# Optimization experiments

Hardware: AMD Instinct MI355X
Metric: run time of the kernel (lower is better)

Reference implementation:

```python
import jax, jax.numpy as jnp
import numpy as np

C = 1024        # number of classes
N = 8           # proxies per class
ALLNUM = C * N  # 8192 total proxies
DIM = 512
R = 0.05
TOPK = int(np.ceil(R * ALLNUM))  # 410
LAM = 0.3
B = 2048


def setup_inputs() -> dict:
    key = jax.random.key(0)
    k1, k2, k3 = jax.random.split(key, 3)
    inp = jax.random.normal(k1, (B, DIM), dtype=jnp.float32)
    target = jax.random.randint(k2, (B,), 0, C, dtype=jnp.int64)
    # kaiming-uniform-initialized proxies approximated by scaled normal init
    proxies = jax.random.normal(k3, (DIM, ALLNUM), dtype=jnp.float32)
    instance_label = jnp.repeat(jnp.arange(C, dtype=jnp.int64), N)  # [ALLNUM]
    return {"input": inp, "target": target, "Proxies": proxies,
            "instance_label": instance_label}


def reference(input, target, Proxies, instance_label):
    # L2-normalize each proxy column (F.normalize along dim=0, eps=1e-12)
    norm = jnp.maximum(jnp.linalg.norm(Proxies, axis=0, keepdims=True), 1e-12)
    centers = Proxies / norm                             # [DIM, ALLNUM]
    similarity = input @ centers                          # [B, ALLNUM]

    positive_mask = (target[:, None] == instance_label[None, :]).astype(similarity.dtype)
    _, indices = jax.lax.top_k(similarity + 1000.0 * positive_mask, TOPK)  # [B, TOPK]

    rows = jnp.arange(similarity.shape[0])[:, None]
    mask = jnp.zeros_like(similarity).at[rows, indices].set(1.0)
    prob_a = mask * similarity                            # sparse-masked similarities

    y_instance_onehot = jax.nn.one_hot(instance_label, C, dtype=similarity.dtype)  # [ALLNUM, C]
    logits = prob_a @ y_instance_onehot                   # [B, C]

    y_target_onehot = jax.nn.one_hot(target, C, dtype=similarity.dtype)  # [B, C]
    logits_mask = 1.0 - (logits == 0.0).astype(similarity.dtype)

    # scale_mask_softmax with scale=1 along dim=1
    e = jnp.exp(logits) * logits_mask
    predict = e / (1e-8 + jnp.sum(e, axis=1, keepdims=True))
    lossClassify = jnp.mean(jnp.sum(-y_target_onehot * jnp.log(predict + 1e-20), axis=1))

    # proxy regularizer: cross-entropy of proxy-vs-class logits
    simCenter = centers.T @ centers                       # [ALLNUM, ALLNUM]
    centers_logits = simCenter @ y_instance_onehot        # [ALLNUM, C]
    logp = jax.nn.log_softmax(centers_logits, axis=1)
    reg = -jnp.mean(jnp.take_along_axis(logp, instance_label[:, None], axis=1))

    return (lossClassify + LAM * reg, lossClassify)
```

## Files before the change

kernel.cpp:

```cpp
#include <hip/hip_runtime.h>
#include <hip/hip_bf16.h>
#include <math.h>

#define C_CLS   1024
#define NPROXY  8
#define ALLNUM  8192
#define DIM     512
#define TOPK    410
#define LAM     0.3f
#define BATCH   2048

#define BAND_CAP_BLK 40
#define ROW_CAP      512
#define GCAP         64

typedef __bf16 bf16x8 __attribute__((ext_vector_type(8)));
typedef float floatx4 __attribute__((ext_vector_type(4)));
typedef unsigned short ushort_t;

#define WS_RNORM 0
#define WS_SIG   8192
#define WS_LP    10240
#define WS_RP    12288
#define WS_CNT   14336
#define WS_NDEF  16384
#define WS_FLAG  18432
#define WS_CLS   20480
#define WS_BVAL  (WS_CLS + 2048*1024)
#define WS_BCOL  (WS_BVAL + 2048*512)
#define WS_ABF   (WS_BCOL + 2048*256)
#define WS_PBF   (WS_ABF + 524288)
#define WS_STBF  (WS_PBF + 2097152)
#define WS_LOG   (WS_STBF + 262144)

__device__ inline float block_reduce(float v, int is_max, float* red, int t) {
    #pragma unroll
    for (int o = 32; o > 0; o >>= 1) {
        float w = __shfl_down(v, o);
        v = is_max ? fmaxf(v, w) : (v + w);
    }
    __syncthreads();
    if ((t & 63) == 0) red[t >> 6] = v;
    __syncthreads();
    return is_max ? fmaxf(fmaxf(red[0], red[1]), fmaxf(red[2], red[3]))
                  : (red[0] + red[1] + red[2] + red[3]);
}

__device__ inline ushort_t f2bf(float f) {
    unsigned u = __float_as_uint(f);
    return (ushort_t)((u + 0x7FFFu + ((u >> 16) & 1u)) >> 16);
}

__device__ inline float bf2f(ushort_t u) {
    return __uint_as_float(((unsigned)u) << 16);
}

__device__ inline void ld_g2l_16(const void* g, void* l) {
    __builtin_amdgcn_global_load_lds(
        (const __attribute__((address_space(1))) unsigned int*)g,
        (__attribute__((address_space(3))) unsigned int*)l,
        16, 0, 0);
}

__device__ inline unsigned f2ord(float f) {
    unsigned u = __float_as_uint(f);
    return (u & 0x80000000u) ? ~u : (u | 0x80000000u);
}

__global__ __launch_bounds__(256) void k_prep1(const float* __restrict__ P,
                                               const float* __restrict__ input,
                                               float* __restrict__ rnorm,
                                               float* __restrict__ rowsig,
                                               ushort_t* __restrict__ Abf,
                                               ushort_t* __restrict__ Pbf,
                                               ushort_t* __restrict__ Stbf,
                                               unsigned* __restrict__ zaux) {
    __shared__ float tile[32][33];
    __shared__ float s_rn[32];
    float* cred = &tile[0][0];
    int bx = blockIdx.x, t = threadIdx.x;
    if (bx < 256) {
        int tc = t & 31, g = t >> 5;
        int c = bx * 32 + tc;
        const float* pc = P + (size_t)(g * 64) * ALLNUM + c;
        float s = 0.f;
        #pragma unroll 8
        for (int d = 0; d < 64; ++d) {
            float v = pc[(size_t)d * ALLNUM];
            s += v * v;
        }
        cred[g * 32 + tc] = s;
        __syncthreads();
        if (g == 0) {
            float tot = 0.f;
            #pragma unroll
            for (int k = 0; k < 8; ++k) tot += cred[k * 32 + tc];
            float r = 1.0f / fmaxf(sqrtf(tot), 1e-12f);
            rnorm[c] = r;
            s_rn[tc] = r;
        }
        __syncthreads();
        #pragma unroll
        for (int p = 0; p < 8; ++p) {
            int idx = t + 256 * p;
            int d = idx >> 2, cc = idx & 3;
            const float* pp = P + (size_t)d * ALLNUM + bx * 32 + cc * 8;
            const float* rr = &s_rn[cc * 8];
            float4 a = *(const float4*)pp;
            float4 b = *(const float4*)(pp + 4);
            float v = a.x * rr[0] + a.y * rr[1] + a.z * rr[2] + a.w * rr[3] +
                      b.x * rr[4] + b.y * rr[5] + b.z * rr[6] + b.w * rr[7];
            Stbf[(size_t)(bx * 4 + cc) * DIM + d] = f2bf(v);
        }
    } else if (bx < 256 + 1024) {
        int a = bx - 256;
        int idx = a * 256 + t;
        float4 v = ((const float4*)input)[idx];
        ushort4 o;
        o.x = f2bf(v.x); o.y = f2bf(v.y); o.z = f2bf(v.z); o.w = f2bf(v.w);
        ((ushort4*)Abf)[idx] = o;
        float sq = v.x * v.x + v.y * v.y + v.z * v.z + v.w * v.w;
        #pragma unroll
        for (int off = 32; off > 0; off >>= 1) sq += __shfl_down(sq, off);
        int lane = t & 63, w = t >> 6;
        if (lane == 0) cred[w] = sq;
        __syncthreads();
        if (t == 0) {
            rowsig[2 * a]     = sqrtf(cred[0] + cred[1]);
            rowsig[2 * a + 1] = sqrtf(cred[2] + cred[3]);
        }
    } else if (bx < 256 + 1024 + 4096) {
        int id = bx - 1280;
        int c0 = (id & 255) * 32, r0 = (id >> 8) * 32;
        int tc = t & 31, tr = t >> 5;
        #pragma unroll
        for (int p = 0; p < 4; ++p)
            tile[tr + p * 8][tc] = P[(size_t)(r0 + tr + p * 8) * ALLNUM + c0 + tc];
        __syncthreads();
        #pragma unroll
        for (int p = 0; p < 4; ++p) {
            int oc = tr + p * 8;
            Pbf[(size_t)(c0 + oc) * DIM + r0 + tc] = f2bf(tile[tc][oc]);
        }
    } else {
        for (int i = t; i < 3 * 2048; i += 256) zaux[i] = 0u;
    }
}

__global__ __launch_bounds__(512, 2) void k_gemms(const ushort_t* __restrict__ Abf,
                                                  const ushort_t* __restrict__ Pbf,
                                                  const ushort_t* __restrict__ Stbf,
                                                  const float* __restrict__ rnorm,
                                                  const float* __restrict__ rowsig,
                                                  const int* __restrict__ target,
                                                  float* __restrict__ g_cls,
                                                  float* __restrict__ g_bval,
                                                  ushort_t* __restrict__ g_bcol,
                                                  unsigned* __restrict__ g_cnt,
                                                  unsigned* __restrict__ g_ndef,
                                                  unsigned* __restrict__ g_flag,
                                                  ushort_t* __restrict__ logits) {
    __shared__ __align__(16) ushort_t smem[65536];
    int bx = blockIdx.x, t = threadIdx.x;
    int w = t >> 6, lane = t & 63;
    int ml = lane & 15, q4 = lane >> 4;

    if (bx < 256) {
        int bi = (bx >> 5) * 256, bj = (bx & 31) * 256;
        int wm = w >> 2, wn = w & 3;
        ushort_t* sA0 = smem;
        ushort_t* sB0 = smem + 16384;
        ushort_t* sA1 = smem + 32768;
        ushort_t* sB1 = smem + 49152;

        floatx4 acc[8][4];
        #pragma unroll
        for (int mf = 0; mf < 8; ++mf)
            #pragma unroll
            for (int nf = 0; nf < 4; ++nf)
                acc[mf][nf] = (floatx4){0.f, 0.f, 0.f, 0.f};

        #define STAGE0(sa, sb, k0) do {                                        \
            _Pragma("unroll")                                                  \
            for (int it = 0; it < 4; ++it) {                                   \
                int c = w * 256 + it * 64 + lane;                              \
                int m = c >> 3, s = c & 7, qq = s ^ (m & 7);                   \
                ld_g2l_16(Abf + ((size_t)(bi + m) << 9) + (k0) + qq * 8,       \
                          &(sa)[c * 8]);                                       \
            }                                                                  \
            _Pragma("unroll")                                                  \
            for (int it = 0; it < 4; ++it) {                                   \
                int c = w * 256 + it * 64 + lane;                              \
                int m = c >> 3, s = c & 7, qq = s ^ (m & 7);                   \
                ld_g2l_16(Pbf + ((size_t)(bj + m) << 9) + (k0) + qq * 8,       \
                          &(sb)[c * 8]);                                       \
            }                                                                  \
        } while (0)

        STAGE0(sA0, sB0, 0);
        __syncthreads();
        #pragma unroll
        for (int tt = 0; tt < 8; ++tt) {
            ushort_t* cA = (tt & 1) ? sA1 : sA0;
            ushort_t* cB = (tt & 1) ? sB1 : sB0;
            if (tt < 7) {
                if (tt & 1) STAGE0(sA0, sB0, (tt + 1) * 64);
                else        STAGE0(sA1, sB1, (tt + 1) * 64);
            }
            #pragma unroll
            for (int kk = 0; kk < 2; ++kk) {
                bf16x8 bfr[4];
                #pragma unroll
                for (int nf = 0; nf < 4; ++nf) {
                    int n = wn * 64 + nf * 16 + ml;
                    int s = (kk * 4 + q4) ^ (n & 7);
                    bfr[nf] = *(const bf16x8*)&cB[n * 64 + s * 8];
                }
                #pragma unroll
                for (int mf = 0; mf < 8; ++mf) {
                    int m = wm * 128 + mf * 16 + ml;
                    int s = (kk * 4 + q4) ^ (m & 7);
                    bf16x8 af = *(const bf16x8*)&cA[m * 64 + s * 8];
                    #pragma unroll
                    for (int nf = 0; nf < 4; ++nf)
                        acc[mf][nf] = __builtin_amdgcn_mfma_f32_16x16x32_bf16(
                            af, bfr[nf], acc[mf][nf], 0, 0, 0);
                }
            }
            __syncthreads();
        }

        unsigned char* sb8 = (unsigned char*)smem;
        float*    e_cls = (float*)sb8;
        float*    e_bv  = (float*)(sb8 + 32768);
        ushort_t* e_bc  = (ushort_t*)(sb8 + 73728);
        unsigned* e_cnt = (unsigned*)(sb8 + 94208);
        unsigned* e_nd  = (unsigned*)(sb8 + 95232);

        #pragma unroll
        for (int i = t; i < 8192; i += 512) e_cls[i] = 0.f;
        if (t < 256) { e_cnt[t] = 0u; e_nd[t] = 0u; }
        __syncthreads();

        #pragma unroll
        for (int mf = 0; mf < 8; ++mf) {
            int rl0 = wm * 128 + mf * 16 + q4 * 4;
            int rowb = bi + rl0;
            float4 rs4 = *(const float4*)&rowsig[rowb];
            int4   tg4 = *(const int4*)&target[rowb];
            #pragma unroll
            for (int nf = 0; nf < 4; ++nf) {
                int cl = wn * 64 + nf * 16 + ml;
                int col = bj + cl;
                float sc = rnorm[col];
                int cls = col >> 3;
                int clsl = cl >> 3;
                #pragma unroll
                for (int i = 0; i < 4; ++i) {
                    int rl = rl0 + i;
                    float v = acc[mf][nf][i] * sc;
                    float sg = ((const float*)&rs4)[i] * (1.0f / 22.616f);
                    float hiT = 1.80f * sg, loT = 1.47f * sg;
                    int tg = ((const int*)&tg4)[i];
                    if (cls == tg) {
                        atomicAdd(&e_cls[rl * 32 + clsl], v);
                    } else if (v >= hiT) {
                        atomicAdd(&e_cls[rl * 32 + clsl], v);
                        atomicAdd(&e_nd[rl], 1u);
                    } else if (v >= loT) {
                        unsigned u = atomicAdd(&e_cnt[rl], 1u);
                        if (u < BAND_CAP_BLK) {
                            e_bv[rl * BAND_CAP_BLK + u] = v;
                            e_bc[rl * BAND_CAP_BLK + u] = (ushort_t)col;
                        }
                    }
                }
            }
        }
        __syncthreads();

        int bjc = bj >> 3;
        #pragma unroll
        for (int i = t; i < 8192; i += 512) {
            int rl = i >> 5, c = i & 31;
            g_cls[(size_t)(bi + rl) * C_CLS + bjc + c] = e_cls[i];
        }
        if (t < 256) {
            int row = bi + t;
            unsigned cbb = e_cnt[t];
            unsigned nd = e_nd[t];
            if (nd) atomicAdd(&g_ndef[row], nd);
            if (cbb) {
                unsigned cc = (cbb > BAND_CAP_BLK) ? BAND_CAP_BLK : cbb;
                unsigned base = atomicAdd(&g_cnt[row], cc);
                if (cbb > BAND_CAP_BLK || base + cc > ROW_CAP) g_flag[row] = 1u;
                for (unsigned j = 0; j < cc; ++j) {
                    if (base + j >= ROW_CAP) break;
                    g_bval[(size_t)row * ROW_CAP + base + j] = e_bv[t * BAND_CAP_BLK + j];
                    g_bcol[(size_t)row * ROW_CAP + base + j] = e_bc[t * BAND_CAP_BLK + j];
                }
            }
        }
        #undef STAGE0
    } else {
        int id = bx - 256;
        int bi = (id >> 3) * 256, bj = (id & 7) * 128;
        int wm = w >> 1, wn = w & 1;
        ushort_t* sA0 = smem;
        ushort_t* sB0 = smem + 16384;
        ushort_t* sA1 = smem + 32768;
        ushort_t* sB1 = smem + 49152;

        floatx4 acc[4][4];
        #pragma unroll
        for (int mf = 0; mf < 4; ++mf)
            #pragma unroll
            for (int nf = 0; nf < 4; ++nf)
                acc[mf][nf] = (floatx4){0.f, 0.f, 0.f, 0.f};

        #define STAGE1(sa, sb, k0) do {                                        \
            _Pragma("unroll")                                                  \
            for (int it = 0; it < 4; ++it) {                                   \
                int c = w * 256 + it * 64 + lane;                              \
                int m = c >> 3, s = c & 7, qq = s ^ (m & 7);                   \
                ld_g2l_16(Pbf + ((size_t)(bi + m) << 9) + (k0) + qq * 8,       \
                          &(sa)[c * 8]);                                       \
            }                                                                  \
            _Pragma("unroll")                                                  \
            for (int it = 0; it < 2; ++it) {                                   \
                int c = w * 128 + it * 64 + lane;                              \
                int m = c >> 3, s = c & 7, qq = s ^ (m & 7);                   \
                ld_g2l_16(Stbf + ((size_t)(bj + m) << 9) + (k0) + qq * 8,      \
                          &(sb)[c * 8]);                                       \
            }                                                                  \
        } while (0)

        STAGE1(sA0, sB0, 0);
        __syncthreads();
        #pragma unroll
        for (int tt = 0; tt < 8; ++tt) {
            ushort_t* cA = (tt & 1) ? sA1 : sA0;
            ushort_t* cB = (tt & 1) ? sB1 : sB0;
            if (tt < 7) {
                if (tt & 1) STAGE1(sA0, sB0, (tt + 1) * 64);
                else        STAGE1(sA1, sB1, (tt + 1) * 64);
            }
            #pragma unroll
            for (int kk = 0; kk < 2; ++kk) {
                bf16x8 bfr[4];
                #pragma unroll
                for (int nf = 0; nf < 4; ++nf) {
                    int n = wn * 64 + nf * 16 + ml;
                    int s = (kk * 4 + q4) ^ (n & 7);
                    bfr[nf] = *(const bf16x8*)&cB[n * 64 + s * 8];
                }
                #pragma unroll
                for (int mf = 0; mf < 4; ++mf) {
                    int m = wm * 64 + mf * 16 + ml;
                    int s = (kk * 4 + q4) ^ (m & 7);
                    bf16x8 af = *(const bf16x8*)&cA[m * 64 + s * 8];
                    #pragma unroll
                    for (int nf = 0; nf < 4; ++nf)
                        acc[mf][nf] = __builtin_amdgcn_mfma_f32_16x16x32_bf16(
                            af, bfr[nf], acc[mf][nf], 0, 0, 0);
                }
            }
            __syncthreads();
        }

        #pragma unroll
        for (int mf = 0; mf < 4; ++mf) {
            int rowb = bi + wm * 64 + mf * 16 + q4 * 4;
            float4 rnr = *(const float4*)&rnorm[rowb];
            #pragma unroll
            for (int nf = 0; nf < 4; ++nf) {
                int col = bj + wn * 64 + nf * 16 + ml;
                #pragma unroll
                for (int i = 0; i < 4; ++i)
                    logits[(size_t)(rowb + i) * C_CLS + col] =
                        f2bf(acc[mf][nf][i] * ((const float*)&rnr)[i]);
            }
        }
        #undef STAGE1
    }
}

__device__ inline void suffix_select1(unsigned* s_hist, unsigned kk,
                                      unsigned* s_wtot, unsigned* sh_bin,
                                      unsigned* sh_k, int t, int lane, int wid) {
    unsigned h = s_hist[t];
    unsigned v = h;
    #pragma unroll
    for (int off = 1; off < 64; off <<= 1) {
        unsigned o = __shfl_down(v, off);
        if (lane + off < 64) v += o;
    }
    if (lane == 0) s_wtot[wid] = v;
    __syncthreads();
    unsigned above = v - h;
    for (int w2 = wid + 1; w2 < 4; ++w2) above += s_wtot[w2];
    unsigned cum = above + h;
    if (cum >= kk && above < kk) { *sh_bin = (unsigned)t; *sh_k = kk - above; }
    __syncthreads();
}

__global__ __launch_bounds__(256) void k_finish(const int* __restrict__ target,
                                                const float* __restrict__ rowsig,
                                                const float* __restrict__ rnorm,
                                                const ushort_t* __restrict__ Abf,
                                                const ushort_t* __restrict__ Pbf,
                                                const float* __restrict__ g_cls,
                                                const float* __restrict__ g_bval,
                                                const ushort_t* __restrict__ g_bcol,
                                                const unsigned* __restrict__ g_cnt,
                                                const unsigned* __restrict__ g_ndef,
                                                const unsigned* __restrict__ g_flag,
                                                float* __restrict__ loss_part,
                                                const ushort_t* __restrict__ logits,
                                                float* __restrict__ reg_part) {
    __shared__ __align__(16) unsigned char smem[16384];
    int bx = blockIdx.x, t = threadIdx.x;
    int lane = t & 63, wid = t >> 6;

    if (bx < 2048) {
        float*    s_cls  = (float*)smem;
        float*    s_bval = (float*)(smem + 4096);
        ushort_t* s_bcol = (ushort_t*)(smem + 6144);
        unsigned* s_hist = (unsigned*)(smem + 7168);
        float*    s_arow = (float*)(smem + 8192);
        unsigned* s_wtot = (unsigned*)(smem + 10240);
        unsigned* shv    = (unsigned*)(smem + 10256);
        float*    shf    = (float*)(smem + 10272);
        float*    red    = (float*)(smem + 10288);
        float*    s_gval = (float*)(smem + 10304);

        int b = bx;
        int tgt = target[b];
        float sig = rowsig[b] * (1.0f / 22.616f);
        float hiT = 1.80f * sig, loT = 1.47f * sig;
        float binscale = 256.0f / (hiT - loT);

        ((float4*)s_cls)[t] = ((const float4*)(g_cls + (size_t)b * C_CLS))[t];
        unsigned cnt = g_cnt[b], nd = g_ndef[b], fl = g_flag[b];
        int kq = (TOPK - NPROXY) - (int)nd;
        int ok = (fl == 0u) && (cnt <= ROW_CAP) && (kq >= 0) && ((int)cnt >= kq);
        if (t == 0) shv[1] = 0u;
        s_hist[t] = 0u;
        __syncthreads();

        if (ok) {
            if (kq > 0) {
                for (int j = t; j < (int)cnt; j += 256) {
                    float v = g_bval[(size_t)b * ROW_CAP + j];
                    s_bval[j] = v;
                    s_bcol[j] = g_bcol[(size_t)b * ROW_CAP + j];
                    int bin = (int)((v - loT) * binscale);
                    bin = (bin > 255) ? 255 : bin;
                    atomicAdd(&s_hist[bin], 1u);
                }
                __syncthreads();
                suffix_select1(s_hist, (unsigned)kq, s_wtot, &shv[2], &shv[3], t, lane, wid);
                int Bb = (int)shv[2];
                int knew = (int)shv[3];
                for (int j = t; j < (int)cnt; j += 256) {
                    float v = s_bval[j];
                    int bin = (int)((v - loT) * binscale);
                    bin = (bin > 255) ? 255 : bin;
                    if (bin == Bb) {
                        unsigned g = atomicAdd(&shv[1], 1u);
                        if (g < GCAP) s_gval[g] = v;
                    }
                }
                __syncthreads();
                int gc = (int)shv[1];
                if (gc <= GCAP) {
                    if (t < gc) {
                        float vj = s_gval[t];
                        unsigned g = 0, geq = 0;
                        for (int i = 0; i < gc; ++i) {
                            float vi = s_gval[i];
                            g   += (vi > vj) ? 1u : 0u;
                            geq += (vi >= vj) ? 1u : 0u;
                        }
                        if (g < (unsigned)knew && geq >= (unsigned)knew) shf[0] = vj;
                    }
                } else {
                    for (int j = t; j < (int)cnt; j += 256) {
                        float vj = s_bval[j];
                        unsigned g = 0, geq = 0;
                        for (int i = 0; i < (int)cnt; ++i) {
                            float vi = s_bval[i];
                            g   += (vi > vj) ? 1u : 0u;
                            geq += (vi >= vj) ? 1u : 0u;
                        }
                        if (g < (unsigned)kq && geq >= (unsigned)kq) shf[0] = vj;
                    }
                }
                __syncthreads();
                float thr = shf[0];
                for (int j = t; j < (int)cnt; j += 256)
                    if (s_bval[j] >= thr)
                        atomicAdd(&s_cls[s_bcol[j] >> 3], s_bval[j]);
            }
        } else {
            for (int i = t; i < DIM; i += 256)
                s_arow[i] = bf2f(Abf[(size_t)b * DIM + i]);
            #pragma unroll
            for (int i = 0; i < 4; ++i) s_cls[t + 256 * i] = 0.f;
            __syncthreads();
            float4 v4[8];
            for (int p = 0; p < 8; ++p) {
                int f = t + 256 * p;
                float vv[4];
                for (int e = 0; e < 4; ++e) {
                    int col = 4 * f + e;
                    const ushort_t* pc = Pbf + (size_t)col * DIM;
                    float a = 0.f;
                    for (int d = 0; d < DIM; ++d)
                        a += s_arow[d] * bf2f(pc[d]);
                    vv[e] = a * rnorm[col];
                }
                float4 o; o.x = vv[0]; o.y = vv[1]; o.z = vv[2]; o.w = vv[3];
                v4[p] = o;
            }
            #pragma unroll
            for (int p = 0; p < 8; ++p) {
                int f = t + 256 * p;
                const float* pv = (const float*)&v4[p];
                if ((f >> 1) == tgt)
                    atomicAdd(&s_cls[tgt], pv[0] + pv[1] + pv[2] + pv[3]);
            }
            unsigned L = 0u, R = 0xFFFFFFFFu;
            for (int it = 0; it < 33 && R - L > 1; ++it) {
                unsigned mid = L + ((R - L) >> 1);
                float c = 0.f;
                #pragma unroll
                for (int p = 0; p < 8; ++p) {
                    int f = t + 256 * p;
                    const float* pv = (const float*)&v4[p];
                    if ((f >> 1) != tgt) {
                        #pragma unroll
                        for (int e = 0; e < 4; ++e)
                            c += (f2ord(pv[e]) >= mid) ? 1.f : 0.f;
                    }
                }
                c = block_reduce(c, 0, red, t);
                if (c >= (float)(TOPK - NPROXY)) L = mid; else R = mid;
                __syncthreads();
            }
            #pragma unroll
            for (int p = 0; p < 8; ++p) {
                int f = t + 256 * p;
                const float* pv = (const float*)&v4[p];
                if ((f >> 1) != tgt) {
                    #pragma unroll
                    for (int e = 0; e < 4; ++e)
                        if (f2ord(pv[e]) >= L)
                            atomicAdd(&s_cls[f >> 1], pv[e]);
                }
            }
        }
        __syncthreads();

        float4 cv = ((const float4*)s_cls)[t];
        float m = -1e30f;
        if (cv.x != 0.0f) m = fmaxf(m, cv.x);
        if (cv.y != 0.0f) m = fmaxf(m, cv.y);
        if (cv.z != 0.0f) m = fmaxf(m, cv.z);
        if (cv.w != 0.0f) m = fmaxf(m, cv.w);
        m = block_reduce(m, 1, red, t);
        float se = 0.f;
        if (cv.x != 0.0f) se += expf(cv.x - m);
        if (cv.y != 0.0f) se += expf(cv.y - m);
        if (cv.z != 0.0f) se += expf(cv.z - m);
        if (cv.w != 0.0f) se += expf(cv.w - m);
        se = block_reduce(se, 0, red, t);
        if (t == 0) {
            float lt = s_cls[tgt];
            float predict_t = expf(lt - m) / (1e-8f * expf(-m) + se);
            loss_part[b] = -logf(predict_t + 1e-20f);
        }
    } else {
        __shared__ float bsum[4];
        int rb = bx - 2048;
        int i = rb * 4 + wid;
        const ushort_t* row = logits + (size_t)i * C_CLS;
        uint4 c0 = ((const uint4*)row)[lane];
        uint4 c1 = ((const uint4*)(row + 512))[lane];

        float f[16];
        const unsigned* u0 = (const unsigned*)&c0;
        const unsigned* u1 = (const unsigned*)&c1;
        #pragma unroll
        for (int k = 0; k < 4; ++k) {
            f[2 * k]     = __uint_as_float(u0[k] << 16);
            f[2 * k + 1] = __uint_as_float(u0[k] & 0xFFFF0000u);
            f[8 + 2 * k]     = __uint_as_float(u1[k] << 16);
            f[8 + 2 * k + 1] = __uint_as_float(u1[k] & 0xFFFF0000u);
        }

        int cstar = i >> 3;
        int chunk = cstar >> 9, within = cstar & 511;
        float sd = 0.f;
        if (lane == (within >> 3)) sd = f[chunk * 8 + (within & 7)];

        float m = -1e30f;
        #pragma unroll
        for (int k = 0; k < 16; ++k) m = fmaxf(m, f[k]);
        #pragma unroll
        for (int off = 32; off > 0; off >>= 1) m = fmaxf(m, __shfl_xor(m, off));

        float se = 0.f;
        #pragma unroll
        for (int k = 0; k < 16; ++k) se += expf(f[k] - m);
        #pragma unroll
        for (int off = 32; off > 0; off >>= 1) se += __shfl_xor(se, off);
        #pragma unroll
        for (int off = 32; off > 0; off >>= 1) sd += __shfl_xor(sd, off);

        if (lane == 0) bsum[wid] = m + logf(se) - sd;
        __syncthreads();
        if (t == 0)
            reg_part[rb] = bsum[0] + bsum[1] + bsum[2] + bsum[3];
    }
}

__global__ __launch_bounds__(256) void k_final(const float* __restrict__ lp,
                                               const float* __restrict__ rp,
                                               float* __restrict__ out) {
    __shared__ float red[4];
    int t = threadIdx.x;
    float4 a = ((const float4*)lp)[t];
    float4 b = ((const float4*)lp)[t + 256];
    float4 c = ((const float4*)rp)[t];
    float4 d = ((const float4*)rp)[t + 256];
    float ls = a.x + a.y + a.z + a.w + b.x + b.y + b.z + b.w;
    float rs = c.x + c.y + c.z + c.w + d.x + d.y + d.z + d.w;
    ls = block_reduce(ls, 0, red, t);
    rs = block_reduce(rs, 0, red, t);
    if (t == 0) {
        float lc = ls / (float)BATCH;
        float rg = rs / (float)ALLNUM;
        out[0] = lc + LAM * rg;
        out[1] = lc;
    }
}

extern "C" void kernel_launch(void* const* d_in, const int* in_sizes, int n_in,
                              void* d_out, int out_size, void* d_ws, size_t ws_size,
                              hipStream_t stream) {
    const float* input  = (const float*)d_in[0];
    const int*   target = (const int*)d_in[1];
    const float* P      = (const float*)d_in[2];

    float* ws        = (float*)d_ws;
    float* rnorm     = ws + WS_RNORM;
    float* rowsig    = ws + WS_SIG;
    float* loss_part = ws + WS_LP;
    float* reg_part  = ws + WS_RP;
    unsigned* g_cnt  = (unsigned*)(ws + WS_CNT);
    unsigned* g_ndef = (unsigned*)(ws + WS_NDEF);
    unsigned* g_flag = (unsigned*)(ws + WS_FLAG);
    float* g_cls     = ws + WS_CLS;
    float* g_bval    = ws + WS_BVAL;
    ushort_t* g_bcol = (ushort_t*)(ws + WS_BCOL);
    ushort_t* Abf    = (ushort_t*)(ws + WS_ABF);
    ushort_t* Pbf    = (ushort_t*)(ws + WS_PBF);
    ushort_t* Stbf   = (ushort_t*)(ws + WS_STBF);
    ushort_t* logits = (ushort_t*)(ws + WS_LOG);
    float* out       = (float*)d_out;

    hipLaunchKernelGGL(k_prep1, dim3(256 + 1024 + 4096 + 1), dim3(256), 0, stream,
                       P, input, rnorm, rowsig, Abf, Pbf, Stbf, g_cnt);
    hipLaunchKernelGGL(k_gemms, dim3(512), dim3(512), 0, stream,
                       Abf, Pbf, Stbf, rnorm, rowsig, target,
                       g_cls, g_bval, g_bcol, g_cnt, g_ndef, g_flag, logits);
    hipLaunchKernelGGL(k_finish, dim3(4096), dim3(256), 0, stream,
                       target, rowsig, rnorm, Abf, Pbf,
                       g_cls, g_bval, g_bcol, g_cnt, g_ndef, g_flag,
                       loss_part, logits, reg_part);
    hipLaunchKernelGGL(k_final, dim3(1), dim3(256), 0, stream,
                       loss_part, reg_part, out);
}
```

Before: 149.1 us.

## Unify both GEMMs into one 256x256 tile path with finer-grained pipelined staging

Both GEMM roles in k_gemms now share one 256x256 tiled main loop. The second GEMM (proxies x class sums) moves from 256x128 tiles over 256 blocks to 256x256 tiles over 128 blocks, so the grid shrinks from 512 to 384. Each k-step is split into four phases that interleave half-tile global-to-LDS loads with MFMA work, raise wave priority around the MFMAs, and wait on outstanding loads only once per step. The first GEMM's block-to-tile mapping is also remapped to improve L2 locality. The aim is better load/compute overlap and more reuse per tile, at the cost of fewer blocks in the second GEMM and more register pressure.

```diff
diff --git a/kernel.cpp b/kernel.cpp
--- a/kernel.cpp
+++ b/kernel.cpp
@@ -164,72 +164,100 @@
     int bx = blockIdx.x, t = threadIdx.x;
     int w = t >> 6, lane = t & 63;
     int ml = lane & 15, q4 = lane >> 4;
-
-    if (bx < 256) {
-        int bi = (bx >> 5) * 256, bj = (bx & 31) * 256;
-        int wm = w >> 2, wn = w & 3;
-        ushort_t* sA0 = smem;
-        ushort_t* sB0 = smem + 16384;
-        ushort_t* sA1 = smem + 32768;
-        ushort_t* sB1 = smem + 49152;
-
-        floatx4 acc[8][4];
-        #pragma unroll
-        for (int mf = 0; mf < 8; ++mf)
-            #pragma unroll
-            for (int nf = 0; nf < 4; ++nf)
-                acc[mf][nf] = (floatx4){0.f, 0.f, 0.f, 0.f};
-
-        #define STAGE0(sa, sb, k0) do {                                        \
-            _Pragma("unroll")                                                  \
-            for (int it = 0; it < 4; ++it) {                                   \
-                int c = w * 256 + it * 64 + lane;                              \
-                int m = c >> 3, s = c & 7, qq = s ^ (m & 7);                   \
-                ld_g2l_16(Abf + ((size_t)(bi + m) << 9) + (k0) + qq * 8,       \
-                          &(sa)[c * 8]);                                       \
-            }                                                                  \
-            _Pragma("unroll")                                                  \
-            for (int it = 0; it < 4; ++it) {                                   \
-                int c = w * 256 + it * 64 + lane;                              \
-                int m = c >> 3, s = c & 7, qq = s ^ (m & 7);                   \
-                ld_g2l_16(Pbf + ((size_t)(bj + m) << 9) + (k0) + qq * 8,       \
-                          &(sb)[c * 8]);                                       \
-            }                                                                  \
-        } while (0)
-
-        STAGE0(sA0, sB0, 0);
-        __syncthreads();
-        #pragma unroll
-        for (int tt = 0; tt < 8; ++tt) {
-            ushort_t* cA = (tt & 1) ? sA1 : sA0;
-            ushort_t* cB = (tt & 1) ? sB1 : sB0;
+    int wm = w >> 2, wn = w & 3;
+
+    int isg0 = (bx < 256);
+    const ushort_t* Ap;
+    const ushort_t* Bp;
+    int bi, bj;
+    if (isg0) {
+        int x_ = bx & 7, r_ = bx >> 3;
+        bi = (r_ >> 2) * 256;
+        bj = (x_ * 4 + (r_ & 3)) * 256;
+        Ap = Abf; Bp = Pbf;
+    } else {
+        int id = bx - 256;
+        bi = (id >> 2) * 256;
+        bj = (id & 3) * 256;
+        Ap = Pbf; Bp = Stbf;
+    }
+
+    floatx4 acc[8][4];
+    #pragma unroll
+    for (int mf = 0; mf < 8; ++mf)
+        #pragma unroll
+        for (int nf = 0; nf < 4; ++nf)
+            acc[mf][nf] = (floatx4){0.f, 0.f, 0.f, 0.f};
+
+    #define STAGE_HALF(Mp, rbase, k0, dstoff) do {                             \
+        _Pragma("unroll")                                                      \
+        for (int it_ = 0; it_ < 2; ++it_) {                                    \
+            int c_ = (it_ * 8 + w) * 64 + lane;                                \
+            int m_ = c_ >> 3, s_ = c_ & 7, q_ = s_ ^ (m_ & 7);                 \
+            ld_g2l_16((Mp) + ((size_t)((rbase) + m_) << 9) + (k0) + q_ * 8,    \
+                      &smem[(dstoff) + c_ * 8]);                               \
+        } } while (0)
+
+    STAGE_HALF(Ap, bi,       0, 0);
+    STAGE_HALF(Ap, bi + 128, 0, 8192);
+    STAGE_HALF(Bp, bj,       0, 16384);
+    STAGE_HALF(Bp, bj + 128, 0, 24576);
+    asm volatile("s_waitcnt vmcnt(0)" ::: "memory");
+    __builtin_amdgcn_s_barrier();
+    asm volatile("" ::: "memory");
+
+    bf16x8 bfr[2][4];
+    #pragma unroll
+    for (int tt = 0; tt < 8; ++tt) {
+        const int Xo = (tt & 1) ? 32768 : 0;
+        const int Yo = 32768 - Xo;
+        const ushort_t* Xa = &smem[Xo];
+        const ushort_t* Xb = &smem[Xo + 16384];
+        #pragma unroll
+        for (int p = 0; p < 4; ++p) {
             if (tt < 7) {
-                if (tt & 1) STAGE0(sA0, sB0, (tt + 1) * 64);
-                else        STAGE0(sA1, sB1, (tt + 1) * 64);
-            }
-            #pragma unroll
-            for (int kk = 0; kk < 2; ++kk) {
-                bf16x8 bfr[4];
+                if (p == 0) STAGE_HALF(Ap, bi,       (tt + 1) * 64, Yo);
+                if (p == 1) STAGE_HALF(Ap, bi + 128, (tt + 1) * 64, Yo + 8192);
+                if (p == 2) STAGE_HALF(Bp, bj,       (tt + 1) * 64, Yo + 16384);
+                if (p == 3) STAGE_HALF(Bp, bj + 128, (tt + 1) * 64, Yo + 24576);
+            }
+            if (p == 0) {
                 #pragma unroll
-                for (int nf = 0; nf < 4; ++nf) {
-                    int n = wn * 64 + nf * 16 + ml;
-                    int s = (kk * 4 + q4) ^ (n & 7);
-                    bfr[nf] = *(const bf16x8*)&cB[n * 64 + s * 8];
-                }
+                for (int kk = 0; kk < 2; ++kk)
+                    #pragma unroll
+                    for (int nf = 0; nf < 4; ++nf) {
+                        int n = wn * 64 + nf * 16 + ml;
+                        int s = (kk * 4 + q4) ^ (n & 7);
+                        bfr[kk][nf] = *(const bf16x8*)&Xb[n * 64 + s * 8];
+                    }
+            }
+            bf16x8 af[2][2];
+            #pragma unroll
+            for (int kk = 0; kk < 2; ++kk)
                 #pragma unroll
-                for (int mf = 0; mf < 8; ++mf) {
-                    int m = wm * 128 + mf * 16 + ml;
+                for (int mi = 0; mi < 2; ++mi) {
+                    int m = wm * 128 + (p * 2 + mi) * 16 + ml;
                     int s = (kk * 4 + q4) ^ (m & 7);
-                    bf16x8 af = *(const bf16x8*)&cA[m * 64 + s * 8];
+                    af[kk][mi] = *(const bf16x8*)&Xa[m * 64 + s * 8];
+                }
+            __builtin_amdgcn_s_setprio(1);
+            #pragma unroll
+            for (int kk = 0; kk < 2; ++kk)
+                #pragma unroll
+                for (int mi = 0; mi < 2; ++mi)
                     #pragma unroll
                     for (int nf = 0; nf < 4; ++nf)
-                        acc[mf][nf] = __builtin_amdgcn_mfma_f32_16x16x32_bf16(
-                            af, bfr[nf], acc[mf][nf], 0, 0, 0);
-                }
-            }
-            __syncthreads();
-        }
-
+                        acc[p * 2 + mi][nf] = __builtin_amdgcn_mfma_f32_16x16x32_bf16(
+                            af[kk][mi], bfr[kk][nf], acc[p * 2 + mi][nf], 0, 0, 0);
+            __builtin_amdgcn_s_setprio(0);
+            if (p == 3) asm volatile("s_waitcnt vmcnt(0)" ::: "memory");
+            __builtin_amdgcn_s_barrier();
+            if (p == 3) asm volatile("" ::: "memory");
+        }
+    }
+    #undef STAGE_HALF
+
+    if (isg0) {
         unsigned char* sb8 = (unsigned char*)smem;
         float*    e_cls = (float*)sb8;
         float*    e_bv  = (float*)(sb8 + 32768);
@@ -301,76 +329,10 @@
                 }
             }
         }
-        #undef STAGE0
     } else {
-        int id = bx - 256;
-        int bi = (id >> 3) * 256, bj = (id & 7) * 128;
-        int wm = w >> 1, wn = w & 1;
-        ushort_t* sA0 = smem;
-        ushort_t* sB0 = smem + 16384;
-        ushort_t* sA1 = smem + 32768;
-        ushort_t* sB1 = smem + 49152;
-
-        floatx4 acc[4][4];
-        #pragma unroll
-        for (int mf = 0; mf < 4; ++mf)
-            #pragma unroll
-            for (int nf = 0; nf < 4; ++nf)
-                acc[mf][nf] = (floatx4){0.f, 0.f, 0.f, 0.f};
-
-        #define STAGE1(sa, sb, k0) do {                                        \
-            _Pragma("unroll")                                                  \
-            for (int it = 0; it < 4; ++it) {                                   \
-                int c = w * 256 + it * 64 + lane;                              \
-                int m = c >> 3, s = c & 7, qq = s ^ (m & 7);                   \
-                ld_g2l_16(Pbf + ((size_t)(bi + m) << 9) + (k0) + qq * 8,       \
-                          &(sa)[c * 8]);                                       \
-            }                                                                  \
-            _Pragma("unroll")                                                  \
-            for (int it = 0; it < 2; ++it) {                                   \
-                int c = w * 128 + it * 64 + lane;                              \
-                int m = c >> 3, s = c & 7, qq = s ^ (m & 7);                   \
-                ld_g2l_16(Stbf + ((size_t)(bj + m) << 9) + (k0) + qq * 8,      \
-                          &(sb)[c * 8]);                                       \
-            }                                                                  \
-        } while (0)
-
-        STAGE1(sA0, sB0, 0);
-        __syncthreads();
-        #pragma unroll
-        for (int tt = 0; tt < 8; ++tt) {
-            ushort_t* cA = (tt & 1) ? sA1 : sA0;
-            ushort_t* cB = (tt & 1) ? sB1 : sB0;
-            if (tt < 7) {
-                if (tt & 1) STAGE1(sA0, sB0, (tt + 1) * 64);
-                else        STAGE1(sA1, sB1, (tt + 1) * 64);
-            }
-            #pragma unroll
-            for (int kk = 0; kk < 2; ++kk) {
-                bf16x8 bfr[4];
-                #pragma unroll
-                for (int nf = 0; nf < 4; ++nf) {
-                    int n = wn * 64 + nf * 16 + ml;
-                    int s = (kk * 4 + q4) ^ (n & 7);
-                    bfr[nf] = *(const bf16x8*)&cB[n * 64 + s * 8];
-                }
-                #pragma unroll
-                for (int mf = 0; mf < 4; ++mf) {
-                    int m = wm * 64 + mf * 16 + ml;
-                    int s = (kk * 4 + q4) ^ (m & 7);
-                    bf16x8 af = *(const bf16x8*)&cA[m * 64 + s * 8];
-                    #pragma unroll
-                    for (int nf = 0; nf < 4; ++nf)
-                        acc[mf][nf] = __builtin_amdgcn_mfma_f32_16x16x32_bf16(
-                            af, bfr[nf], acc[mf][nf], 0, 0, 0);
-                }
-            }
-            __syncthreads();
-        }
-
-        #pragma unroll
-        for (int mf = 0; mf < 4; ++mf) {
-            int rowb = bi + wm * 64 + mf * 16 + q4 * 4;
+        #pragma unroll
+        for (int mf = 0; mf < 8; ++mf) {
+            int rowb = bi + wm * 128 + mf * 16 + q4 * 4;
             float4 rnr = *(const float4*)&rnorm[rowb];
             #pragma unroll
             for (int nf = 0; nf < 4; ++nf) {
@@ -381,7 +343,6 @@
                         f2bf(acc[mf][nf][i] * ((const float*)&rnr)[i]);
             }
         }
-        #undef STAGE1
     }
 }
 
@@ -672,7 +633,7 @@
 
     hipLaunchKernelGGL(k_prep1, dim3(256 + 1024 + 4096 + 1), dim3(256), 0, stream,
                        P, input, rnorm, rowsig, Abf, Pbf, Stbf, g_cnt);
-    hipLaunchKernelGGL(k_gemms, dim3(512), dim3(512), 0, stream,
+    hipLaunchKernelGGL(k_gemms, dim3(384), dim3(512), 0, stream,
                        Abf, Pbf, Stbf, rnorm, rowsig, target,
                        g_cls, g_bval, g_bcol, g_cnt, g_ndef, g_flag, logits);
     hipLaunchKernelGGL(k_finish, dim3(4096), dim3(256), 0, stream,
```

Measured after the change: 152.7 us. 2.5% more time.
